# Kernel optimization log

Hardware: AMD Instinct MI355X
Metric: run time of the kernel (lower is better)

The kernel has to match this reference:

```python
import jax, jax.numpy as jnp
import numpy as np

N_NODES = 100000
N_EDGES = 1600000
FEAT = 128
EMB = 128
N_ROOTS = 4096


def _gcn_layer(x, W, b, src, dst, n):
    # PyG GCNConv(add_self_loops=False, normalize=False):
    # h = x @ W; out_i = sum_{j in N(i)} h_j ; out = out + bias
    h = x @ W                                  # [N_in, EMB]
    msgs = h[src]                              # gather per edge [E, EMB]
    return jax.ops.segment_sum(msgs, dst, num_segments=n) + b


def setup_inputs() -> dict:
    key = jax.random.key(0)
    k = jax.random.split(key, 10)
    x = jax.random.normal(k[0], (N_NODES, FEAT), dtype=jnp.float32)
    edge_index = jax.random.randint(k[1], (2, N_EDGES), 0, N_NODES, dtype=jnp.int64 if jax.config.jax_enable_x64 else jnp.int32)
    root_mask = jnp.zeros((N_NODES,), dtype=bool).at[:N_ROOTS].set(True)
    s0 = 1.0 / np.sqrt(FEAT)
    s1 = 1.0 / np.sqrt(FEAT + EMB)
    W0 = jax.random.normal(k[2], (FEAT, EMB), dtype=jnp.float32) * s0
    W1 = jax.random.normal(k[3], (EMB + FEAT, EMB), dtype=jnp.float32) * s1
    W2 = jax.random.normal(k[4], (EMB + FEAT, EMB), dtype=jnp.float32) * s1
    W3 = jax.random.normal(k[5], (EMB + FEAT, EMB), dtype=jnp.float32) * s1
    b0 = jnp.zeros((EMB,), jnp.float32)
    b1 = jnp.zeros((EMB,), jnp.float32)
    b2 = jnp.zeros((EMB,), jnp.float32)
    b3 = jnp.zeros((EMB,), jnp.float32)
    return {"x": x, "edge_index": edge_index, "root_mask": root_mask, "num_roots": N_ROOTS,
            "W0": W0, "b0": b0, "W1": W1, "b1": b1, "W2": W2, "b2": b2, "W3": W3, "b3": b3}


def reference(x, edge_index, root_mask, num_roots, W0, b0, W1, b1, W2, b2, W3, b3):
    src, dst = edge_index[0], edge_index[1]
    n = x.shape[0]
    h = _gcn_layer(x, W0, b0, src, dst, n)
    for W, b in ((W1, b1), (W2, b2), (W3, b3)):
        prev = h
        inp = jnp.concatenate((jax.nn.relu(h), x), axis=1)  # concat_initial_features
        h = prev + _gcn_layer(inp, W, b, src, dst, n)        # residual
    roots = jnp.nonzero(root_mask, size=num_roots)[0]
    return h[roots]
```

## Files before the change

kernel.cpp:

```cpp
#include <hip/hip_runtime.h>
#include <hip/hip_bf16.h>
#include <stdint.h>

#define N_NODES 100000
#define N_EDGES 1600000
#define FEAT 128
#define EMB 128
#define N_ROOTS 4096

#define BUCKET_BITS 9
#define BUCKET_NODES 512
#define NBUCK ((N_NODES + BUCKET_NODES - 1) / BUCKET_NODES)
#define BUCK_CAP 12288
#define BIN_CHUNK 4096
#define NB_BIN ((N_EDGES + BIN_CHUNK - 1) / BIN_CHUNK)
#define BUCK_SLACK 4096
#define SRCS_CAP (N_EDGES + NBUCK * BUCK_SLACK + 4096)

typedef __attribute__((ext_vector_type(4))) float f32x4;
typedef __attribute__((ext_vector_type(8))) short bf16x8;

__device__ __forceinline__ ushort f2b(float f) {
  uint32_t u = __float_as_uint(f);
  uint32_t r = (u + 0x7FFFu + ((u >> 16) & 1u)) >> 16;
  return (ushort)r;
}

__global__ void k_cvt_bf16(const float* __restrict__ in, ushort* __restrict__ out, int n4) {
  int i = blockIdx.x * blockDim.x + threadIdx.x;
  int stride = gridDim.x * blockDim.x;
  for (; i < n4; i += stride) {
    float4 v = ((const float4*)in)[i];
    ushort4 o;
    o.x = f2b(v.x); o.y = f2b(v.y); o.z = f2b(v.z); o.w = f2b(v.w);
    ((ushort4*)out)[i] = o;
  }
}

__global__ void k_cvtW(const float* __restrict__ W, ushort* __restrict__ Wswz, int K) {
  int idx = blockIdx.x * blockDim.x + threadIdx.x;
  if (idx >= K * 128) return;
  int k = idx >> 7, c = idx & 127;
  ushort b = f2b(W[idx]);
  *(ushort*)((char*)Wswz + c * (K * 2) + ((k * 2) ^ ((c & 7) << 4))) = b;
}

__global__ __launch_bounds__(256) void k_bin(const int* __restrict__ srcA, const int* __restrict__ dstA,
                                             int* __restrict__ bucket_cnt, int* __restrict__ binned) {
  __shared__ int hist[NBUCK];
  __shared__ int lscan[NBUCK];
  __shared__ int rsv[NBUCK];
  __shared__ int lpos[NBUCK];
  __shared__ int ws[4];
  __shared__ int2 ent[BIN_CHUNK];
  int t = threadIdx.x;
  int e0 = blockIdx.x * BIN_CHUNK;
  int cnt = min(BIN_CHUNK, N_EDGES - e0);
  for (int i = t; i < NBUCK; i += 256) hist[i] = 0;
  __syncthreads();
  for (int j = t; j < cnt; j += 256) atomicAdd(&hist[dstA[e0 + j] >> BUCKET_BITS], 1);
  __syncthreads();
  {
    int lane = t & 63, wv = t >> 6;
    int v = (t < NBUCK) ? hist[t] : 0;
    int inc = v;
    for (int d = 1; d < 64; d <<= 1) { int x = __shfl_up(inc, d); if (lane >= d) inc += x; }
    if (lane == 63) ws[wv] = inc;
    __syncthreads();
    int wbase = 0;
    for (int k = 0; k < wv; ++k) wbase += ws[k];
    if (t < NBUCK) {
      int excl = wbase + inc - v;
      lscan[t] = excl;
      lpos[t] = excl;
      rsv[t] = (v > 0) ? atomicAdd(&bucket_cnt[t], v) : 0;
    }
  }
  __syncthreads();
  for (int j = t; j < cnt; j += 256) {
    int s = srcA[e0 + j], d = dstA[e0 + j];
    int p = atomicAdd(&lpos[d >> BUCKET_BITS], 1);
    ent[p] = make_int2(s, d);
  }
  __syncthreads();
  for (int j = t; j < cnt; j += 256) {
    int2 E = ent[j];
    int b = E.y >> BUCKET_BITS;
    int pos = rsv[b] + (j - lscan[b]);
    if (pos < BUCK_CAP)
      binned[b * BUCK_CAP + pos] = (E.x << BUCKET_BITS) | (E.y & (BUCKET_NODES - 1));
  }
}

__global__ __launch_bounds__(256) void k_bucket_scan(const int* __restrict__ bucket_cnt,
                                                     int* __restrict__ bucket_base) {
  __shared__ int ws[4];
  int t = threadIdx.x;
  int lane = t & 63, wv = t >> 6;
  int v = (t < NBUCK) ? bucket_cnt[t] : 0;
  int inc = v;
  for (int d = 1; d < 64; d <<= 1) { int x = __shfl_up(inc, d); if (lane >= d) inc += x; }
  if (lane == 63) ws[wv] = inc;
  __syncthreads();
  int wbase = 0;
  for (int k = 0; k < wv; ++k) wbase += ws[k];
  if (t < NBUCK) bucket_base[t] = (wbase + inc - v) + t * BUCK_SLACK;
}

__global__ __launch_bounds__(512) void k_csr(const int* __restrict__ binned,
                                             const int* __restrict__ bucket_cnt,
                                             const int* __restrict__ bucket_base,
                                             int2* __restrict__ off2, int* __restrict__ srcs) {
  __shared__ int deg[BUCKET_NODES];
  __shared__ int sAb[BUCKET_NODES];
  __shared__ int sBb[BUCKET_NODES];
  __shared__ int pos[BUCKET_NODES];
  __shared__ int epk[BUCK_CAP];
  int b = blockIdx.x;
  int t = threadIdx.x;
  int cnt = min(bucket_cnt[b], BUCK_CAP);
  int gbase = bucket_base[b];
  int n0 = b * BUCKET_NODES;
  int nn = min(BUCKET_NODES, N_NODES - n0);
  deg[t] = 0;
  __syncthreads();
  for (int j = t; j < cnt; j += 512) {
    int p = binned[b * BUCK_CAP + j];
    epk[j] = p;
    atomicAdd(&deg[p & (BUCKET_NODES - 1)], 1);
  }
  __syncthreads();
  int d = deg[t];
  int dp = (d + 7) & ~7;
  int* sA = sAb; int* sB = sBb;
  sA[t] = dp;
  __syncthreads();
  for (int q = 1; q < 512; q <<= 1) {
    int x = sA[t];
    if (t >= q) x += sA[t - q];
    sB[t] = x;
    __syncthreads();
    int* tp = sA; sA = sB; sB = tp;
  }
  int ex = sA[t] - dp;
  pos[t] = ex;
  if (t < nn) off2[n0 + t] = make_int2(gbase + ex, gbase + ex + dp);
  __syncthreads();
  for (int j = t; j < cnt; j += 512) {
    int p = epk[j];
    int q = atomicAdd(&pos[p & (BUCKET_NODES - 1)], 1);
    srcs[gbase + q] = p >> BUCKET_BITS;
  }
  __syncthreads();
  for (int q = ex + d; q < ex + dp; ++q) srcs[gbase + q] = N_NODES;
}

__global__ __launch_bounds__(256) void k_gemm(
    const ushort* __restrict__ A0, const ushort* __restrict__ A1,
    const ushort* __restrict__ Wswz, ushort* __restrict__ out, int n, int K, int relu0)
{
  extern __shared__ char smem[];
  int bytes = K * 256;
  for (int idx = threadIdx.x * 16; idx < bytes; idx += 256 * 16)
    *(uint4*)(smem + idx) = *(const uint4*)((const char*)Wswz + idx);
  __syncthreads();

  int lane = threadIdx.x & 63;
  int wv = threadIdx.x >> 6;
  int rowBase = blockIdx.x * 128 + wv * 32;
  int rl = lane & 15;
  int kh = lane >> 4;
  int r0 = rowBase + rl, r1 = r0 + 16;
  int r0c = min(r0, n - 1), r1c = min(r1, n - 1);

  f32x4 acc[2][8];
#pragma unroll
  for (int i = 0; i < 2; ++i)
#pragma unroll
    for (int j = 0; j < 8; ++j)
      acc[i][j] = (f32x4){0.f, 0.f, 0.f, 0.f};

  int nks = K >> 5;
  bf16x8 a0, a1;
  {
    const ushort* Asrc = A0;
    int kof = (kh << 3);
    a0 = *(const bf16x8*)(Asrc + (size_t)r0c * 128 + kof);
    a1 = *(const bf16x8*)(Asrc + (size_t)r1c * 128 + kof);
  }
  for (int ks = 0; ks < nks; ++ks) {
    bf16x8 na0 = a0, na1 = a1;
    if (ks + 1 < nks) {
      int ksn = ks + 1;
      const ushort* Asrc = (ksn < 4) ? A0 : A1;
      int kof = ((ksn & 3) << 5) + (kh << 3);
      na0 = *(const bf16x8*)(Asrc + (size_t)r0c * 128 + kof);
      na1 = *(const bf16x8*)(Asrc + (size_t)r1c * 128 + kof);
    }
    if (relu0 && ks < 4) {
#pragma unroll
      for (int q = 0; q < 8; ++q) {
        short v0 = a0[q]; a0[q] = (short)(v0 & ~(v0 >> 15));
        short v1 = a1[q]; a1[q] = (short)(v1 & ~(v1 >> 15));
      }
    }
    int kk = (ks << 5) + (kh << 3);
#pragma unroll
    for (int ct = 0; ct < 8; ++ct) {
      int col = (ct << 4) + rl;
      bf16x8 b = *(const bf16x8*)(smem + col * (K * 2) + ((kk * 2) ^ ((col & 7) << 4)));
      acc[0][ct] = __builtin_amdgcn_mfma_f32_16x16x32_bf16(a0, b, acc[0][ct], 0, 0, 0);
      acc[1][ct] = __builtin_amdgcn_mfma_f32_16x16x32_bf16(a1, b, acc[1][ct], 0, 0, 0);
    }
    a0 = na0; a1 = na1;
  }
#pragma unroll
  for (int ri = 0; ri < 2; ++ri)
#pragma unroll
    for (int ct = 0; ct < 8; ++ct) {
      int col = (ct << 4) + rl;
#pragma unroll
      for (int j = 0; j < 4; ++j) {
        int row = rowBase + ri * 16 + kh * 4 + j;
        if (row < n) out[(size_t)row * 128 + col] = f2b(acc[ri][ct][j]);
      }
    }
}

__global__ __launch_bounds__(256) void k_aggr(
    const ushort* __restrict__ hlin, const int2* __restrict__ off2, const int* __restrict__ srcs,
    const float* __restrict__ bias, ushort* __restrict__ hbf, float* __restrict__ outf,
    int n, int first, int last)
{
  int node = blockIdx.x * 4 + (threadIdx.x >> 6);
  if (node >= n) return;
  int lane = threadIdx.x & 63;
  int2 se = off2[node];
  int s = __builtin_amdgcn_readfirstlane(se.x);
  int e = __builtin_amdgcn_readfirstlane(se.y);
  float a0 = 0.f, a1 = 0.f;
  int j = s;
  for (; j + 16 <= e; j += 16) {
    int ix[16];
#pragma unroll
    for (int q = 0; q < 16; ++q) ix[q] = srcs[j + q];
    uint32_t u[16];
#pragma unroll
    for (int q = 0; q < 16; ++q)
      u[q] = *(const uint32_t*)(hlin + (size_t)ix[q] * 128 + lane * 2);
#pragma unroll
    for (int q = 0; q < 16; ++q) {
      a0 += __uint_as_float(u[q] << 16);
      a1 += __uint_as_float(u[q] & 0xFFFF0000u);
    }
  }
  if (j < e) {
    int ix[8];
#pragma unroll
    for (int q = 0; q < 8; ++q) ix[q] = srcs[j + q];
    uint32_t u[8];
#pragma unroll
    for (int q = 0; q < 8; ++q)
      u[q] = *(const uint32_t*)(hlin + (size_t)ix[q] * 128 + lane * 2);
#pragma unroll
    for (int q = 0; q < 8; ++q) {
      a0 += __uint_as_float(u[q] << 16);
      a1 += __uint_as_float(u[q] & 0xFFFF0000u);
    }
  }
  float2 bv = ((const float2*)bias)[lane];
  size_t idx = (size_t)node * 128 + lane * 2;
  float h0, h1;
  if (first) {
    h0 = a0 + bv.x; h1 = a1 + bv.y;
  } else {
    uint32_t up = *(const uint32_t*)(hbf + idx);
    h0 = __uint_as_float(up << 16) + a0 + bv.x;
    h1 = __uint_as_float(up & 0xFFFF0000u) + a1 + bv.y;
  }
  if (last) {
    *(float2*)(outf + idx) = make_float2(h0, h1);
  } else {
    ushort2 r; r.x = f2b(h0); r.y = f2b(h1);
    *(ushort2*)(hbf + idx) = r;
  }
}

extern "C" void kernel_launch(void* const* d_in, const int* in_sizes, int n_in,
                              void* d_out, int out_size, void* d_ws, size_t ws_size,
                              hipStream_t stream) {
  const float* x = (const float*)d_in[0];
  const int* ei  = (const int*)d_in[1];
  const int* src = ei;
  const int* dst = ei + N_EDGES;
  const float* Wp[4] = {(const float*)d_in[4], (const float*)d_in[6],
                        (const float*)d_in[8], (const float*)d_in[10]};
  const float* bp[4] = {(const float*)d_in[5], (const float*)d_in[7],
                        (const float*)d_in[9], (const float*)d_in[11]};
  const int Kl[4] = {128, 256, 256, 256};

  char* w = (char*)d_ws;
  auto alloc = [&](size_t bytes) {
    char* p = w;
    w += (bytes + 255) & ~(size_t)255;
    return p;
  };
  ushort* x_bf     = (ushort*)alloc((size_t)N_NODES * 128 * 2);
  ushort* hbf      = (ushort*)alloc((size_t)N_NODES * 128 * 2);
  ushort* hlin     = (ushort*)alloc((size_t)(N_NODES + 8) * 128 * 2);
  int2*   off2     = (int2*)  alloc((size_t)N_NODES * 8);
  int*    srcs     = (int*)   alloc((size_t)SRCS_CAP * 4);
  int*    binned   = (int*)   alloc((size_t)NBUCK * BUCK_CAP * 4);
  int*    bucket_cnt  = (int*)alloc((size_t)NBUCK * 4);
  int*    bucket_base = (int*)alloc((size_t)NBUCK * 4);
  ushort* Wswz[4];
  for (int l = 0; l < 4; ++l) Wswz[l] = (ushort*)alloc((size_t)Kl[l] * 128 * 2);
  if ((size_t)(w - (char*)d_ws) > ws_size) return;

  hipMemsetAsync(bucket_cnt, 0, (size_t)NBUCK * 4, stream);
  hipMemsetAsync(hlin + (size_t)N_NODES * 128, 0, 256, stream);
  k_cvt_bf16<<<2048, 256, 0, stream>>>(x, x_bf, N_NODES * 128 / 4);
  for (int l = 0; l < 4; ++l)
    k_cvtW<<<(Kl[l] * 128 + 255) / 256, 256, 0, stream>>>(Wp[l], Wswz[l], Kl[l]);
  k_bin<<<NB_BIN, 256, 0, stream>>>(src, dst, bucket_cnt, binned);
  k_bucket_scan<<<1, 256, 0, stream>>>(bucket_cnt, bucket_base);
  k_csr<<<NBUCK, 512, 0, stream>>>(binned, bucket_cnt, bucket_base, off2, srcs);

  int gblocks = (N_NODES + 127) / 128;
  int ablocks = (N_NODES + 3) / 4;
  k_gemm<<<gblocks, 256, 128 * 128 * 2, stream>>>(x_bf, x_bf, Wswz[0], hlin, N_NODES, 128, 0);
  k_aggr<<<ablocks, 256, 0, stream>>>(hlin, off2, srcs, bp[0], hbf, (float*)d_out, N_NODES, 1, 0);
  for (int l = 1; l < 4; ++l) {
    k_gemm<<<gblocks, 256, 256 * 128 * 2, stream>>>(hbf, x_bf, Wswz[l], hlin, N_NODES, 256, 1);
    if (l < 3) {
      k_aggr<<<ablocks, 256, 0, stream>>>(hlin, off2, srcs, bp[l], hbf, (float*)d_out,
                                          N_NODES, 0, 0);
    } else {
      k_aggr<<<(N_ROOTS + 3) / 4, 256, 0, stream>>>(hlin, off2, srcs, bp[l], hbf, (float*)d_out,
                                                    N_ROOTS, 0, 1);
    }
  }
}
```

Measured before the change: 345.6 us.

## Aggregate before transform and reuse aggregated input features across layers

Uses linearity to reorder each GCN layer from gather(XW) to (gathered X)W. The aggregated raw features are computed once and reused by every layer's concat, and ReLU is applied inside the gather. Bias and residual are fused into the GEMM epilogue. Because of the reorder, the last layer's GEMM only needs to run on the root rows instead of all nodes. The cost is an extra bf16 rounding of the aggregated sums before the matmul, which may change numerical accuracy.

```diff
diff --git a/kernel.cpp b/kernel.cpp
--- a/kernel.cpp
+++ b/kernel.cpp
@@ -155,82 +155,9 @@
   for (int q = ex + d; q < ex + dp; ++q) srcs[gbase + q] = N_NODES;
 }
 
-__global__ __launch_bounds__(256) void k_gemm(
-    const ushort* __restrict__ A0, const ushort* __restrict__ A1,
-    const ushort* __restrict__ Wswz, ushort* __restrict__ out, int n, int K, int relu0)
-{
-  extern __shared__ char smem[];
-  int bytes = K * 256;
-  for (int idx = threadIdx.x * 16; idx < bytes; idx += 256 * 16)
-    *(uint4*)(smem + idx) = *(const uint4*)((const char*)Wswz + idx);
-  __syncthreads();
-
-  int lane = threadIdx.x & 63;
-  int wv = threadIdx.x >> 6;
-  int rowBase = blockIdx.x * 128 + wv * 32;
-  int rl = lane & 15;
-  int kh = lane >> 4;
-  int r0 = rowBase + rl, r1 = r0 + 16;
-  int r0c = min(r0, n - 1), r1c = min(r1, n - 1);
-
-  f32x4 acc[2][8];
-#pragma unroll
-  for (int i = 0; i < 2; ++i)
-#pragma unroll
-    for (int j = 0; j < 8; ++j)
-      acc[i][j] = (f32x4){0.f, 0.f, 0.f, 0.f};
-
-  int nks = K >> 5;
-  bf16x8 a0, a1;
-  {
-    const ushort* Asrc = A0;
-    int kof = (kh << 3);
-    a0 = *(const bf16x8*)(Asrc + (size_t)r0c * 128 + kof);
-    a1 = *(const bf16x8*)(Asrc + (size_t)r1c * 128 + kof);
-  }
-  for (int ks = 0; ks < nks; ++ks) {
-    bf16x8 na0 = a0, na1 = a1;
-    if (ks + 1 < nks) {
-      int ksn = ks + 1;
-      const ushort* Asrc = (ksn < 4) ? A0 : A1;
-      int kof = ((ksn & 3) << 5) + (kh << 3);
-      na0 = *(const bf16x8*)(Asrc + (size_t)r0c * 128 + kof);
-      na1 = *(const bf16x8*)(Asrc + (size_t)r1c * 128 + kof);
-    }
-    if (relu0 && ks < 4) {
-#pragma unroll
-      for (int q = 0; q < 8; ++q) {
-        short v0 = a0[q]; a0[q] = (short)(v0 & ~(v0 >> 15));
-        short v1 = a1[q]; a1[q] = (short)(v1 & ~(v1 >> 15));
-      }
-    }
-    int kk = (ks << 5) + (kh << 3);
-#pragma unroll
-    for (int ct = 0; ct < 8; ++ct) {
-      int col = (ct << 4) + rl;
-      bf16x8 b = *(const bf16x8*)(smem + col * (K * 2) + ((kk * 2) ^ ((col & 7) << 4)));
-      acc[0][ct] = __builtin_amdgcn_mfma_f32_16x16x32_bf16(a0, b, acc[0][ct], 0, 0, 0);
-      acc[1][ct] = __builtin_amdgcn_mfma_f32_16x16x32_bf16(a1, b, acc[1][ct], 0, 0, 0);
-    }
-    a0 = na0; a1 = na1;
-  }
-#pragma unroll
-  for (int ri = 0; ri < 2; ++ri)
-#pragma unroll
-    for (int ct = 0; ct < 8; ++ct) {
-      int col = (ct << 4) + rl;
-#pragma unroll
-      for (int j = 0; j < 4; ++j) {
-        int row = rowBase + ri * 16 + kh * 4 + j;
-        if (row < n) out[(size_t)row * 128 + col] = f2b(acc[ri][ct][j]);
-      }
-    }
-}
-
 __global__ __launch_bounds__(256) void k_aggr(
-    const ushort* __restrict__ hlin, const int2* __restrict__ off2, const int* __restrict__ srcs,
-    const float* __restrict__ bias, ushort* __restrict__ hbf, float* __restrict__ outf,
-    int n, int first, int last)
+    const ushort* __restrict__ table, const int2* __restrict__ off2, const int* __restrict__ srcs,
+    ushort* __restrict__ outagg, int n, int relu)
 {
   int node = blockIdx.x * 4 + (threadIdx.x >> 6);
   if (node >= n) return;
@@ -247,9 +174,10 @@
     uint32_t u[16];
 #pragma unroll
     for (int q = 0; q < 16; ++q)
-      u[q] = *(const uint32_t*)(hlin + (size_t)ix[q] * 128 + lane * 2);
+      u[q] = *(const uint32_t*)(table + (size_t)ix[q] * 128 + lane * 2);
 #pragma unroll
     for (int q = 0; q < 16; ++q) {
+      if (relu) { uint32_t m = (u[q] >> 15) & 0x00010001u; u[q] &= ~(m * 0xFFFFu); }
       a0 += __uint_as_float(u[q] << 16);
       a1 += __uint_as_float(u[q] & 0xFFFF0000u);
     }
@@ -261,29 +189,93 @@
     uint32_t u[8];
 #pragma unroll
     for (int q = 0; q < 8; ++q)
-      u[q] = *(const uint32_t*)(hlin + (size_t)ix[q] * 128 + lane * 2);
+      u[q] = *(const uint32_t*)(table + (size_t)ix[q] * 128 + lane * 2);
 #pragma unroll
     for (int q = 0; q < 8; ++q) {
+      if (relu) { uint32_t m = (u[q] >> 15) & 0x00010001u; u[q] &= ~(m * 0xFFFFu); }
       a0 += __uint_as_float(u[q] << 16);
       a1 += __uint_as_float(u[q] & 0xFFFF0000u);
     }
   }
-  float2 bv = ((const float2*)bias)[lane];
-  size_t idx = (size_t)node * 128 + lane * 2;
-  float h0, h1;
-  if (first) {
-    h0 = a0 + bv.x; h1 = a1 + bv.y;
-  } else {
-    uint32_t up = *(const uint32_t*)(hbf + idx);
-    h0 = __uint_as_float(up << 16) + a0 + bv.x;
-    h1 = __uint_as_float(up & 0xFFFF0000u) + a1 + bv.y;
-  }
-  if (last) {
-    *(float2*)(outf + idx) = make_float2(h0, h1);
-  } else {
-    ushort2 r; r.x = f2b(h0); r.y = f2b(h1);
-    *(ushort2*)(hbf + idx) = r;
-  }
+  uint32_t pk = (uint32_t)f2b(a0) | ((uint32_t)f2b(a1) << 16);
+  *(uint32_t*)(outagg + (size_t)node * 128 + lane * 2) = pk;
+}
+
+__global__ __launch_bounds__(256) void k_gemm(
+    const ushort* __restrict__ A0, const ushort* __restrict__ A1,
+    const ushort* __restrict__ Wswz, const ushort* __restrict__ resid,
+    const float* __restrict__ bias,
+    ushort* __restrict__ outb, float* __restrict__ outf, int n, int K)
+{
+  extern __shared__ char smem[];
+  int bytes = K * 256;
+  for (int idx = threadIdx.x * 16; idx < bytes; idx += 256 * 16)
+    *(uint4*)(smem + idx) = *(const uint4*)((const char*)Wswz + idx);
+  __syncthreads();
+
+  int lane = threadIdx.x & 63;
+  int wv = threadIdx.x >> 6;
+  int rowBase = blockIdx.x * 128 + wv * 32;
+  int rl = lane & 15;
+  int kh = lane >> 4;
+  int r0 = rowBase + rl, r1 = r0 + 16;
+  int r0c = min(r0, n - 1), r1c = min(r1, n - 1);
+
+  f32x4 acc[2][8];
+#pragma unroll
+  for (int i = 0; i < 2; ++i)
+#pragma unroll
+    for (int j = 0; j < 8; ++j)
+      acc[i][j] = (f32x4){0.f, 0.f, 0.f, 0.f};
+
+  int nks = K >> 5;
+  bf16x8 a0, a1;
+  {
+    int kof = (kh << 3);
+    a0 = *(const bf16x8*)(A0 + (size_t)r0c * 128 + kof);
+    a1 = *(const bf16x8*)(A0 + (size_t)r1c * 128 + kof);
+  }
+  for (int ks = 0; ks < nks; ++ks) {
+    bf16x8 na0 = a0, na1 = a1;
+    if (ks + 1 < nks) {
+      int ksn = ks + 1;
+      const ushort* Asrc = (ksn < 4) ? A0 : A1;
+      int kof = ((ksn & 3) << 5) + (kh << 3);
+      na0 = *(const bf16x8*)(Asrc + (size_t)r0c * 128 + kof);
+      na1 = *(const bf16x8*)(Asrc + (size_t)r1c * 128 + kof);
+    }
+    int kk = (ks << 5) + (kh << 3);
+#pragma unroll
+    for (int ct = 0; ct < 8; ++ct) {
+      int col = (ct << 4) + rl;
+      bf16x8 b = *(const bf16x8*)(smem + col * (K * 2) + ((kk * 2) ^ ((col & 7) << 4)));
+      acc[0][ct] = __builtin_amdgcn_mfma_f32_16x16x32_bf16(a0, b, acc[0][ct], 0, 0, 0);
+      acc[1][ct] = __builtin_amdgcn_mfma_f32_16x16x32_bf16(a1, b, acc[1][ct], 0, 0, 0);
+    }
+    a0 = na0; a1 = na1;
+  }
+  float bv[8];
+#pragma unroll
+  for (int ct = 0; ct < 8; ++ct) bv[ct] = bias[(ct << 4) + rl];
+#pragma unroll
+  for (int ri = 0; ri < 2; ++ri)
+#pragma unroll
+    for (int ct = 0; ct < 8; ++ct) {
+      int col = (ct << 4) + rl;
+#pragma unroll
+      for (int j = 0; j < 4; ++j) {
+        int row = rowBase + ri * 16 + kh * 4 + j;
+        if (row < n) {
+          float v = acc[ri][ct][j] + bv[ct];
+          if (resid) {
+            ushort rr = resid[(size_t)row * 128 + col];
+            v += __uint_as_float(((uint32_t)rr) << 16);
+          }
+          if (outf) outf[(size_t)row * 128 + col] = v;
+          else outb[(size_t)row * 128 + col] = f2b(v);
+        }
+      }
+    }
 }
 
 extern "C" void kernel_launch(void* const* d_in, const int* in_sizes, int n_in,
@@ -305,12 +297,13 @@
     w += (bytes + 255) & ~(size_t)255;
     return p;
   };
-  ushort* x_bf     = (ushort*)alloc((size_t)N_NODES * 128 * 2);
-  ushort* hbf      = (ushort*)alloc((size_t)N_NODES * 128 * 2);
-  ushort* hlin     = (ushort*)alloc((size_t)(N_NODES + 8) * 128 * 2);
-  int2*   off2     = (int2*)  alloc((size_t)N_NODES * 8);
-  int*    srcs     = (int*)   alloc((size_t)SRCS_CAP * 4);
-  int*    binned   = (int*)   alloc((size_t)NBUCK * BUCK_CAP * 4);
+  ushort* x_bf  = (ushort*)alloc((size_t)(N_NODES + 8) * 128 * 2);
+  ushort* hbf   = (ushort*)alloc((size_t)(N_NODES + 8) * 128 * 2);
+  ushort* xagg  = (ushort*)alloc((size_t)N_NODES * 128 * 2);
+  ushort* ragg  = (ushort*)alloc((size_t)N_NODES * 128 * 2);
+  int2*   off2  = (int2*)  alloc((size_t)N_NODES * 8);
+  int*    srcs  = (int*)   alloc((size_t)SRCS_CAP * 4);
+  int*    binned = (int*)  alloc((size_t)NBUCK * BUCK_CAP * 4);
   int*    bucket_cnt  = (int*)alloc((size_t)NBUCK * 4);
   int*    bucket_base = (int*)alloc((size_t)NBUCK * 4);
   ushort* Wswz[4];
@@ -318,7 +311,8 @@
   if ((size_t)(w - (char*)d_ws) > ws_size) return;
 
   hipMemsetAsync(bucket_cnt, 0, (size_t)NBUCK * 4, stream);
-  hipMemsetAsync(hlin + (size_t)N_NODES * 128, 0, 256, stream);
+  hipMemsetAsync(x_bf + (size_t)N_NODES * 128, 0, 256, stream);
+  hipMemsetAsync(hbf + (size_t)N_NODES * 128, 0, 256, stream);
   k_cvt_bf16<<<2048, 256, 0, stream>>>(x, x_bf, N_NODES * 128 / 4);
   for (int l = 0; l < 4; ++l)
     k_cvtW<<<(Kl[l] * 128 + 255) / 256, 256, 0, stream>>>(Wp[l], Wswz[l], Kl[l]);
@@ -326,18 +320,20 @@
   k_bucket_scan<<<1, 256, 0, stream>>>(bucket_cnt, bucket_base);
   k_csr<<<NBUCK, 512, 0, stream>>>(binned, bucket_cnt, bucket_base, off2, srcs);
 
-  int gblocks = (N_NODES + 127) / 128;
-  int ablocks = (N_NODES + 3) / 4;
-  k_gemm<<<gblocks, 256, 128 * 128 * 2, stream>>>(x_bf, x_bf, Wswz[0], hlin, N_NODES, 128, 0);
-  k_aggr<<<ablocks, 256, 0, stream>>>(hlin, off2, srcs, bp[0], hbf, (float*)d_out, N_NODES, 1, 0);
-  for (int l = 1; l < 4; ++l) {
-    k_gemm<<<gblocks, 256, 256 * 128 * 2, stream>>>(hbf, x_bf, Wswz[l], hlin, N_NODES, 256, 1);
-    if (l < 3) {
-      k_aggr<<<ablocks, 256, 0, stream>>>(hlin, off2, srcs, bp[l], hbf, (float*)d_out,
-                                          N_NODES, 0, 0);
-    } else {
-      k_aggr<<<(N_ROOTS + 3) / 4, 256, 0, stream>>>(hlin, off2, srcs, bp[l], hbf, (float*)d_out,
-                                                    N_ROOTS, 0, 1);
-    }
-  }
-}
+  int gfull = (N_NODES + 127) / 128;
+  int groot = (N_ROOTS + 127) / 128;
+  int afull = (N_NODES + 3) / 4;
+  int aroot = (N_ROOTS + 3) / 4;
+
+  k_aggr<<<afull, 256, 0, stream>>>(x_bf, off2, srcs, xagg, N_NODES, 0);
+  k_gemm<<<gfull, 256, 128 * 128 * 2, stream>>>(xagg, xagg, Wswz[0], nullptr, bp[0],
+                                                hbf, nullptr, N_NODES, 128);
+  for (int l = 1; l < 3; ++l) {
+    k_aggr<<<afull, 256, 0, stream>>>(hbf, off2, srcs, ragg, N_NODES, 1);
+    k_gemm<<<gfull, 256, 256 * 128 * 2, stream>>>(ragg, xagg, Wswz[l], hbf, bp[l],
+                                                  hbf, nullptr, N_NODES, 256);
+  }
+  k_aggr<<<aroot, 256, 0, stream>>>(hbf, off2, srcs, ragg, N_ROOTS, 1);
+  k_gemm<<<groot, 256, 256 * 128 * 2, stream>>>(ragg, xagg, Wswz[3], hbf, bp[3],
+                                                nullptr, (float*)d_out, N_ROOTS, 256);
+}
```

Result: slower. 398.8 us (+15.4%).

## Restrict last-layer GEMM and prior aggregation to roots' receptive field

Applied to the files above, without the earlier changes.

Marks the root nodes and their in-neighbours, then compacts them into a list using per-bucket counts, a scan and a scatter. The layer-2 aggregation and layer-3 GEMM process only the listed nodes, skipping rows that cannot affect the root outputs. This adds several small preprocessing kernels and indirect row gathers in the GEMM. It relies on the fixed structure where only root rows are returned.

```diff
diff --git a/kernel.cpp b/kernel.cpp
--- a/kernel.cpp
+++ b/kernel.cpp
@@ -155,10 +155,82 @@
   for (int q = ex + d; q < ex + dp; ++q) srcs[gbase + q] = N_NODES;
 }
 
+__global__ __launch_bounds__(256) void k_flag(const int2* __restrict__ off2,
+                                              const int* __restrict__ srcs, int* __restrict__ flag) {
+  int root = blockIdx.x * 4 + (threadIdx.x >> 6);
+  if (root >= N_ROOTS) return;
+  int lane = threadIdx.x & 63;
+  if (lane == 0) flag[root] = 1;
+  int2 se = off2[root];
+  for (int j = se.x + lane; j < se.y; j += 64) flag[srcs[j]] = 1;
+}
+
+__global__ __launch_bounds__(512) void k_scnt(const int* __restrict__ flag, int* __restrict__ bcnt) {
+  __shared__ int ws[8];
+  int b = blockIdx.x, t = threadIdx.x;
+  int n0 = b * BUCKET_NODES;
+  int nn = min(BUCKET_NODES, N_NODES - n0);
+  int f = (t < nn) ? flag[n0 + t] : 0;
+  int lane = t & 63, wv = t >> 6;
+  int s = f;
+  for (int q = 1; q < 64; q <<= 1) s += __shfl_xor(s, q);
+  if (lane == 0) ws[wv] = s;
+  __syncthreads();
+  if (t == 0) {
+    int tot = 0;
+    for (int k = 0; k < 8; ++k) tot += ws[k];
+    bcnt[b] = tot;
+  }
+}
+
+__global__ __launch_bounds__(256) void k_sscan(const int* __restrict__ bcnt,
+                                               int* __restrict__ bbase, int* __restrict__ cntP) {
+  __shared__ int ws[4];
+  int t = threadIdx.x;
+  int lane = t & 63, wv = t >> 6;
+  int v = (t < NBUCK) ? bcnt[t] : 0;
+  int inc = v;
+  for (int d = 1; d < 64; d <<= 1) { int x = __shfl_up(inc, d); if (lane >= d) inc += x; }
+  if (lane == 63) ws[wv] = inc;
+  __syncthreads();
+  int wbase = 0;
+  for (int k = 0; k < wv; ++k) wbase += ws[k];
+  if (t < NBUCK) bbase[t] = wbase + inc - v;
+  if (t == NBUCK - 1) *cntP = wbase + inc;
+}
+
+__global__ __launch_bounds__(512) void k_sscat(const int* __restrict__ flag,
+                                               const int* __restrict__ bbase, int* __restrict__ list) {
+  __shared__ int sAb[BUCKET_NODES];
+  __shared__ int sBb[BUCKET_NODES];
+  int b = blockIdx.x, t = threadIdx.x;
+  int n0 = b * BUCKET_NODES;
+  int nn = min(BUCKET_NODES, N_NODES - n0);
+  int f = (t < nn) ? flag[n0 + t] : 0;
+  int* sA = sAb; int* sB = sBb;
+  sA[t] = f;
+  __syncthreads();
+  for (int q = 1; q < 512; q <<= 1) {
+    int x = sA[t];
+    if (t >= q) x += sA[t - q];
+    sB[t] = x;
+    __syncthreads();
+    int* tp = sA; sA = sB; sB = tp;
+  }
+  if (f) list[bbase[b] + sA[t] - 1] = n0 + t;
+}
+
 __global__ __launch_bounds__(256) void k_gemm(
     const ushort* __restrict__ A0, const ushort* __restrict__ A1,
-    const ushort* __restrict__ Wswz, ushort* __restrict__ out, int n, int K, int relu0)
+    const ushort* __restrict__ Wswz, ushort* __restrict__ out,
+    const int* __restrict__ list, const int* __restrict__ cntP,
+    int n, int K, int relu0)
 {
+  int nEff = n;
+  if (list) {
+    nEff = *cntP;
+    if (blockIdx.x * 128 >= nEff) return;
+  }
   extern __shared__ char smem[];
   int bytes = K * 256;
   for (int idx = threadIdx.x * 16; idx < bytes; idx += 256 * 16)
@@ -170,8 +242,9 @@
   int rowBase = blockIdx.x * 128 + wv * 32;
   int rl = lane & 15;
   int kh = lane >> 4;
-  int r0 = rowBase + rl, r1 = r0 + 16;
-  int r0c = min(r0, n - 1), r1c = min(r1, n - 1);
+  int r0 = min(rowBase + rl, nEff - 1), r1 = min(rowBase + rl + 16, nEff - 1);
+  int n0 = list ? list[r0] : r0;
+  int n1 = list ? list[r1] : r1;
 
   f32x4 acc[2][8];
 #pragma unroll
@@ -183,10 +256,9 @@
   int nks = K >> 5;
   bf16x8 a0, a1;
   {
-    const ushort* Asrc = A0;
     int kof = (kh << 3);
-    a0 = *(const bf16x8*)(Asrc + (size_t)r0c * 128 + kof);
-    a1 = *(const bf16x8*)(Asrc + (size_t)r1c * 128 + kof);
+    a0 = *(const bf16x8*)(A0 + (size_t)n0 * 128 + kof);
+    a1 = *(const bf16x8*)(A0 + (size_t)n1 * 128 + kof);
   }
   for (int ks = 0; ks < nks; ++ks) {
     bf16x8 na0 = a0, na1 = a1;
@@ -194,8 +266,8 @@
       int ksn = ks + 1;
       const ushort* Asrc = (ksn < 4) ? A0 : A1;
       int kof = ((ksn & 3) << 5) + (kh << 3);
-      na0 = *(const bf16x8*)(Asrc + (size_t)r0c * 128 + kof);
-      na1 = *(const bf16x8*)(Asrc + (size_t)r1c * 128 + kof);
+      na0 = *(const bf16x8*)(Asrc + (size_t)n0 * 128 + kof);
+      na1 = *(const bf16x8*)(Asrc + (size_t)n1 * 128 + kof);
     }
     if (relu0 && ks < 4) {
 #pragma unroll
@@ -222,7 +294,10 @@
 #pragma unroll
       for (int j = 0; j < 4; ++j) {
         int row = rowBase + ri * 16 + kh * 4 + j;
-        if (row < n) out[(size_t)row * 128 + col] = f2b(acc[ri][ct][j]);
+        if (row < nEff) {
+          int orow = list ? list[row] : row;
+          out[(size_t)orow * 128 + col] = f2b(acc[ri][ct][j]);
+        }
       }
     }
 }
@@ -230,10 +305,19 @@
 __global__ __launch_bounds__(256) void k_aggr(
     const ushort* __restrict__ hlin, const int2* __restrict__ off2, const int* __restrict__ srcs,
     const float* __restrict__ bias, ushort* __restrict__ hbf, float* __restrict__ outf,
+    const int* __restrict__ list, const int* __restrict__ cntP,
     int n, int first, int last)
 {
-  int node = blockIdx.x * 4 + (threadIdx.x >> 6);
-  if (node >= n) return;
+  int gid = blockIdx.x * 4 + (threadIdx.x >> 6);
+  int node;
+  if (list) {
+    int cnt = *cntP;
+    if (gid >= cnt) return;
+    node = list[gid];
+  } else {
+    if (gid >= n) return;
+    node = gid;
+  }
   int lane = threadIdx.x & 63;
   int2 se = off2[node];
   int s = __builtin_amdgcn_readfirstlane(se.x);
@@ -313,11 +397,17 @@
   int*    binned   = (int*)   alloc((size_t)NBUCK * BUCK_CAP * 4);
   int*    bucket_cnt  = (int*)alloc((size_t)NBUCK * 4);
   int*    bucket_base = (int*)alloc((size_t)NBUCK * 4);
+  int*    flag     = (int*)   alloc((size_t)(N_NODES + 1) * 4);
+  int*    slist    = (int*)   alloc((size_t)N_NODES * 4);
+  int*    sbcnt    = (int*)   alloc((size_t)NBUCK * 4);
+  int*    sbbase   = (int*)   alloc((size_t)NBUCK * 4);
+  int*    scnt     = (int*)   alloc(256);
   ushort* Wswz[4];
   for (int l = 0; l < 4; ++l) Wswz[l] = (ushort*)alloc((size_t)Kl[l] * 128 * 2);
   if ((size_t)(w - (char*)d_ws) > ws_size) return;
 
   hipMemsetAsync(bucket_cnt, 0, (size_t)NBUCK * 4, stream);
+  hipMemsetAsync(flag, 0, (size_t)(N_NODES + 1) * 4, stream);
   hipMemsetAsync(hlin + (size_t)N_NODES * 128, 0, 256, stream);
   k_cvt_bf16<<<2048, 256, 0, stream>>>(x, x_bf, N_NODES * 128 / 4);
   for (int l = 0; l < 4; ++l)
@@ -325,19 +415,27 @@
   k_bin<<<NB_BIN, 256, 0, stream>>>(src, dst, bucket_cnt, binned);
   k_bucket_scan<<<1, 256, 0, stream>>>(bucket_cnt, bucket_base);
   k_csr<<<NBUCK, 512, 0, stream>>>(binned, bucket_cnt, bucket_base, off2, srcs);
+  k_flag<<<(N_ROOTS + 3) / 4, 256, 0, stream>>>(off2, srcs, flag);
+  k_scnt<<<NBUCK, 512, 0, stream>>>(flag, sbcnt);
+  k_sscan<<<1, 256, 0, stream>>>(sbcnt, sbbase, scnt);
+  k_sscat<<<NBUCK, 512, 0, stream>>>(flag, sbbase, slist);
 
   int gblocks = (N_NODES + 127) / 128;
   int ablocks = (N_NODES + 3) / 4;
-  k_gemm<<<gblocks, 256, 128 * 128 * 2, stream>>>(x_bf, x_bf, Wswz[0], hlin, N_NODES, 128, 0);
-  k_aggr<<<ablocks, 256, 0, stream>>>(hlin, off2, srcs, bp[0], hbf, (float*)d_out, N_NODES, 1, 0);
-  for (int l = 1; l < 4; ++l) {
-    k_gemm<<<gblocks, 256, 256 * 128 * 2, stream>>>(hbf, x_bf, Wswz[l], hlin, N_NODES, 256, 1);
-    if (l < 3) {
-      k_aggr<<<ablocks, 256, 0, stream>>>(hlin, off2, srcs, bp[l], hbf, (float*)d_out,
-                                          N_NODES, 0, 0);
-    } else {
-      k_aggr<<<(N_ROOTS + 3) / 4, 256, 0, stream>>>(hlin, off2, srcs, bp[l], hbf, (float*)d_out,
-                                                    N_ROOTS, 0, 1);
-    }
-  }
-}
+  k_gemm<<<gblocks, 256, 128 * 256, stream>>>(x_bf, x_bf, Wswz[0], hlin,
+                                              nullptr, nullptr, N_NODES, 128, 0);
+  k_aggr<<<ablocks, 256, 0, stream>>>(hlin, off2, srcs, bp[0], hbf, (float*)d_out,
+                                      nullptr, nullptr, N_NODES, 1, 0);
+  k_gemm<<<gblocks, 256, 256 * 256, stream>>>(hbf, x_bf, Wswz[1], hlin,
+                                              nullptr, nullptr, N_NODES, 256, 1);
+  k_aggr<<<ablocks, 256, 0, stream>>>(hlin, off2, srcs, bp[1], hbf, (float*)d_out,
+                                      nullptr, nullptr, N_NODES, 0, 0);
+  k_gemm<<<gblocks, 256, 256 * 256, stream>>>(hbf, x_bf, Wswz[2], hlin,
+                                              nullptr, nullptr, N_NODES, 256, 1);
+  k_aggr<<<ablocks, 256, 0, stream>>>(hlin, off2, srcs, bp[2], hbf, (float*)d_out,
+                                      slist, scnt, N_NODES, 0, 0);
+  k_gemm<<<gblocks, 256, 256 * 256, stream>>>(hbf, x_bf, Wswz[3], hlin,
+                                              slist, scnt, N_NODES, 256, 1);
+  k_aggr<<<(N_ROOTS + 3) / 4, 256, 0, stream>>>(hlin, off2, srcs, bp[3], hbf, (float*)d_out,
+                                                nullptr, nullptr, N_ROOTS, 0, 1);
+}
```

Result: slower. 361.3 us (+4.6%).
